# Performance work log

Measured on AMD Instinct MI355X. Metric: run time of the kernel, lower is better.

Reference implementation:

```python
import jax, jax.numpy as jnp
import numpy as np

B, N, C = 4, 2048, 512
H, D, L = 8, 64, 64  # num_heads, per-head dim, lunchbox_dim
SCALE = max(D, L) ** (-0.5)

def setup_inputs() -> dict:
    key = jax.random.key(0)
    k1, k2, k3, k4 = jax.random.split(key, 4)
    x = jax.random.normal(k1, (B, N, C), dtype=jnp.float32)
    v = jax.random.normal(k2, (N, H, L), dtype=jnp.float32) * (1.0 / np.sqrt(N))
    qkv = jax.random.normal(k3, (C, D * 2 * H), dtype=jnp.float32) * (1.0 / np.sqrt(C))
    proj = jax.random.normal(k4, (H * L, D), dtype=jnp.float32) * (1.0 / np.sqrt(H * L))
    return {"x": x, "v": v, "qkv": qkv, "proj": proj}

def reference(x, v, qkv, proj):
    # x: [B,N,C] -> [B,N,H,2,D]
    h = jnp.einsum('bnc,cd->bnd', x, qkv).reshape(B, N, H, 2, D)
    q = h[:, :, :, 0, :]  # [B,N,H,D]
    k = h[:, :, :, 1, :]  # [B,N,H,D]
    # attention scores [B,H,N,N]; NOTE: original code calls tf.nn.softmax but
    # discards the result, so no softmax is applied (faithful reproduction).
    attn = jnp.einsum('bnhd,bmhd->bhnm', q, k) * SCALE
    # contract with batch-independent lunchbox V: [B,H,N,N] x [N,H,L] -> [B,N,H,L]
    res = jnp.einsum('bhnm,mhl->bnhl', attn, v).reshape(B, N, H * L)
    out = jnp.einsum('bnc,cd->bnd', res, proj)  # [B,N,D]
    return out
```

## Files before the change

### kernel.cpp

```cpp
#include <hip/hip_runtime.h>
#include <hip/hip_bf16.h>


using f32x4 = __attribute__((ext_vector_type(4))) float;
using s16x8 = __attribute__((ext_vector_type(8))) short;

__device__ __forceinline__ unsigned short f2bf(float f) {
  unsigned int i;
  __builtin_memcpy(&i, &f, 4);
  unsigned int lsb = (i >> 16) & 1u;
  i += 0x7fffu + lsb;
  return (unsigned short)(i >> 16);
}
__device__ __forceinline__ float bf2f(unsigned short u) {
  unsigned int i = ((unsigned int)u) << 16;
  float f;
  __builtin_memcpy(&f, &i, 4);
  return f;
}
__device__ __forceinline__ ushort4 pk4(f32x4 a) {
  ushort4 u;
  u.x = f2bf(a[0]); u.y = f2bf(a[1]); u.z = f2bf(a[2]); u.w = f2bf(a[3]);
  return u;
}
__device__ __forceinline__ void async_cp16(const void* g, void* l) {
  __builtin_amdgcn_global_load_lds((const __attribute__((address_space(1))) void*)g,
                                   (__attribute__((address_space(3))) void*)l, 16, 0, 0);
}

__global__ void k_prep(const float* __restrict__ qkv, unsigned short* __restrict__ qkvT) {
  __shared__ float tile[32][33];
  const int idx = blockIdx.x;
  const int tid = threadIdx.x;
  const int j0 = (idx & 31) * 32;
  const int c0 = (idx >> 5) * 32;
  const int tx = tid & 31, ty = tid >> 5;
#pragma unroll
  for (int i = 0; i < 32; i += 8)
    tile[ty + i][tx] = qkv[(size_t)(c0 + ty + i) * 1024 + j0 + tx];
  __syncthreads();
  const int h = j0 >> 7, s = (j0 >> 6) & 1, d0 = j0 & 63;
  const int jp0 = s * 512 + h * 64 + d0;
#pragma unroll
  for (int i = 0; i < 32; i += 8)
    qkvT[(size_t)(jp0 + ty + i) * 512 + c0 + tx] = f2bf(tile[tx][ty + i]);
}

__global__ __launch_bounds__(512) void k_gemm1(
    const float* __restrict__ X,
    const unsigned short* __restrict__ Bt,
    unsigned short* __restrict__ Qws,
    unsigned short* __restrict__ Kws) {
  __shared__ unsigned short As[128 * 80];
  __shared__ unsigned short Bs[128 * 64];
  const int lin = blockIdx.x;
  const int wg = (lin & 7) * 64 + (lin >> 3);
  const int m0 = (wg >> 3) * 128;
  const int n0 = (wg & 7) * 128;
  const int tid = threadIdx.x;
  const int lane = tid & 63;
  const int wave = tid >> 6;
  const int wm = wave >> 1, wn = wave & 1;

  f32x4 acc[2][4] = {};

  const int arow_s = tid >> 4;
  const int acol_s = (tid & 15) * 4;
  const int rlane = lane >> 3;
  const int clane = (lane & 7) * 8;

  f32x4 areg[4];
#pragma unroll
  for (int i = 0; i < 4; ++i)
    areg[i] = *(const f32x4*)(X + (size_t)(m0 + i * 32 + arow_s) * 512 + acol_s);

  for (int kt = 0; kt < 512; kt += 64) {
    __syncthreads();
#pragma unroll
    for (int i = 0; i < 2; ++i)
      async_cp16(Bt + (size_t)(n0 + i * 64 + wave * 8 + rlane) * 512 + kt + clane,
                 Bs + (i * 64 + wave * 8) * 64);
#pragma unroll
    for (int i = 0; i < 4; ++i)
      *(ushort4*)(As + (i * 32 + arow_s) * 80 + acol_s) = pk4(areg[i]);
    __syncthreads();
    if (kt + 64 < 512) {
#pragma unroll
      for (int i = 0; i < 4; ++i)
        areg[i] = *(const f32x4*)(X + (size_t)(m0 + i * 32 + arow_s) * 512 + kt + 64 + acol_s);
    }
#pragma unroll
    for (int kk = 0; kk < 64; kk += 32) {
      s16x8 af[2], bfr[4];
#pragma unroll
      for (int i = 0; i < 2; ++i)
        af[i] = *(const s16x8*)(As + (wm * 32 + i * 16 + (lane & 15)) * 80 + kk + (lane >> 4) * 8);
#pragma unroll
      for (int j = 0; j < 4; ++j)
        bfr[j] = *(const s16x8*)(Bs + (wn * 64 + j * 16 + (lane & 15)) * 64 + kk + (lane >> 4) * 8);
#pragma unroll
      for (int i = 0; i < 2; ++i)
#pragma unroll
        for (int j = 0; j < 4; ++j)
          acc[i][j] = __builtin_amdgcn_mfma_f32_16x16x32_bf16(af[i], bfr[j], acc[i][j], 0, 0, 0);
    }
  }
  const int n_base = n0 + wn * 64;
#pragma unroll
  for (int i = 0; i < 2; ++i) {
    int grow = m0 + wm * 32 + i * 16 + (lane >> 4) * 4;
#pragma unroll
    for (int j = 0; j < 4; ++j) {
      int gcol = n_base + j * 16 + (lane & 15);
      unsigned short* dst;
      float scale;
      if (gcol < 512) { dst = Qws; scale = 0.125f; }
      else            { dst = Kws; gcol -= 512; scale = 1.0f; }
#pragma unroll
      for (int r = 0; r < 4; ++r)
        dst[(size_t)(grow + r) * 512 + gcol] = f2bf(acc[i][j][r] * scale);
    }
  }
}

__global__ void k_kv_partial(const unsigned short* __restrict__ Kws,
                             const float* __restrict__ v,
                             unsigned short* __restrict__ KVp) {
  const int wg = blockIdx.x;
  const int chunk = wg & 15;
  const int h = (wg >> 4) & 7;
  const int b = wg >> 7;
  __shared__ unsigned short Ks[128 * 64];
  __shared__ float Vs[128 * 64];
  const int tid = threadIdx.x;
  const int lane = tid & 63;
  const int wave = tid >> 6;
  const int n0 = chunk * 128;
  {
    const int r = wave * 32 + (lane >> 3);
    const int c = (lane & 7) * 8;
#pragma unroll
    for (int i = 0; i < 4; ++i)
      async_cp16(Kws + (size_t)(b * 2048 + n0 + r + i * 8) * 512 + h * 64 + c,
                 Ks + (wave * 32 + i * 8) * 64);
  }
  {
    const int r = wave * 32 + (lane >> 4);
    const int c = (lane & 15) * 4;
#pragma unroll
    for (int i = 0; i < 8; ++i)
      async_cp16(v + (size_t)(n0 + r + i * 4) * 512 + h * 64 + c,
                 Vs + (wave * 32 + i * 4) * 64);
  }
  __syncthreads();
  const int dq0 = (tid & 15) * 4;
  const int l0 = (tid >> 4) * 4;
  float acc[4][4] = {};
#pragma unroll 4
  for (int n = 0; n < 128; ++n) {
    ushort4 ku = *(const ushort4*)(Ks + n * 64 + dq0);
    f32x4 va = *(const f32x4*)(Vs + n * 64 + l0);
    float ka[4] = {bf2f(ku.x), bf2f(ku.y), bf2f(ku.z), bf2f(ku.w)};
#pragma unroll
    for (int a = 0; a < 4; ++a)
#pragma unroll
      for (int c = 0; c < 4; ++c)
        acc[a][c] += ka[a] * va[c];
  }
  unsigned short* dst = KVp + (size_t)wg * 4096;
#pragma unroll
  for (int a = 0; a < 4; ++a) {
    f32x4 o;
    o[0] = acc[a][0]; o[1] = acc[a][1]; o[2] = acc[a][2]; o[3] = acc[a][3];
    *(ushort4*)(dst + (dq0 + a) * 64 + l0) = pk4(o);
  }
}

__global__ void k_w(const unsigned short* __restrict__ KVp,
                    const float* __restrict__ proj,
                    unsigned short* __restrict__ WcatT) {
  const int blk = blockIdx.x;
  const int g = blk & 7;
  const int bh = blk >> 3;
  const int h = bh & 7;
  const int b = bh >> 3;
  __shared__ float kv[8 * 64];
  __shared__ float pj[64 * 64];
  const int tid = threadIdx.x;
  {
    const int e = tid * 2;
    const unsigned short* src = KVp + (size_t)bh * 16 * 4096 + g * 512 + e;
    float s0 = 0.f, s1 = 0.f;
#pragma unroll
    for (int c = 0; c < 16; ++c) {
      ushort2 t = *(const ushort2*)(src + c * 4096);
      s0 += bf2f(t.x); s1 += bf2f(t.y);
    }
    kv[e] = s0; kv[e + 1] = s1;
  }
#pragma unroll
  for (int j = 0; j < 16; ++j) {
    int e = tid + j * 256;
    pj[e] = proj[(size_t)h * 4096 + e];
  }
  __syncthreads();
  const int dout = tid & 63;
  const int dq0 = tid >> 6;
  float w0 = 0.f, w1 = 0.f;
  for (int l = 0; l < 64; ++l) {
    float p = pj[l * 64 + dout];
    w0 += kv[dq0 * 64 + l] * p;
    w1 += kv[(dq0 + 4) * 64 + l] * p;
  }
  const int dqb = h * 64 + g * 8;
  WcatT[(size_t)(b * 64 + dout) * 512 + dqb + dq0] = f2bf(w0);
  WcatT[(size_t)(b * 64 + dout) * 512 + dqb + dq0 + 4] = f2bf(w1);
}

__global__ __launch_bounds__(64) void k_gemm2(
    const unsigned short* __restrict__ Qws,
    const unsigned short* __restrict__ WcatT,
    float* __restrict__ out) {
  const int m0 = blockIdx.x * 16;
  const int lane = threadIdx.x;
  const unsigned short* Bb = WcatT + (size_t)(m0 >> 11) * 64 * 512;
  const int arow = lane & 15;
  const int koff = (lane >> 4) * 8;
  f32x4 acc[4] = {};
#pragma unroll
  for (int kk = 0; kk < 16; ++kk) {
    s16x8 af = *(const s16x8*)(Qws + (size_t)(m0 + arow) * 512 + kk * 32 + koff);
#pragma unroll
    for (int j = 0; j < 4; ++j) {
      s16x8 bf = *(const s16x8*)(Bb + (size_t)(j * 16 + arow) * 512 + kk * 32 + koff);
      acc[j] = __builtin_amdgcn_mfma_f32_16x16x32_bf16(af, bf, acc[j], 0, 0, 0);
    }
  }
  const int grow = m0 + (lane >> 4) * 4;
#pragma unroll
  for (int j = 0; j < 4; ++j) {
    int gcol = j * 16 + arow;
#pragma unroll
    for (int r = 0; r < 4; ++r)
      out[(size_t)(grow + r) * 64 + gcol] = acc[j][r];
  }
}

extern "C" void kernel_launch(void* const* d_in, const int* in_sizes, int n_in,
                              void* d_out, int out_size, void* d_ws, size_t ws_size,
                              hipStream_t stream) {
  const float* x    = (const float*)d_in[0];
  const float* v    = (const float*)d_in[1];
  const float* qkv  = (const float*)d_in[2];
  const float* proj = (const float*)d_in[3];
  float* out = (float*)d_out;

  char* ws = (char*)d_ws;
  unsigned short* qkvT = (unsigned short*)ws; ws += (size_t)1024 * 512 * 2;
  unsigned short* Qws  = (unsigned short*)ws; ws += (size_t)8192 * 512 * 2;
  unsigned short* Kws  = (unsigned short*)ws; ws += (size_t)8192 * 512 * 2;
  unsigned short* KVp  = (unsigned short*)ws; ws += (size_t)512 * 4096 * 2;
  unsigned short* Wc   = (unsigned short*)ws; ws += (size_t)4 * 64 * 512 * 2;

  hipLaunchKernelGGL(k_prep, dim3(512), dim3(256), 0, stream, qkv, qkvT);
  hipLaunchKernelGGL(k_gemm1, dim3(512), dim3(512), 0, stream, x, qkvT, Qws, Kws);
  hipLaunchKernelGGL(k_kv_partial, dim3(512), dim3(256), 0, stream, Kws, v, KVp);
  hipLaunchKernelGGL(k_w, dim3(256), dim3(256), 0, stream, KVp, proj, Wc);
  hipLaunchKernelGGL(k_gemm2, dim3(512), dim3(64), 0, stream, Qws, Wc, out);
}
```

Baseline: 112.1 us.

## Double-buffer B tile and prefetch two stages ahead in QKV GEMM

Restructures the k_gemm1 main loop so the bf16 B tile is double-buffered in LDS and loaded two k-steps ahead, while the fp32 A tile is also prefetched two steps ahead into registers. Explicit s_waitcnt vmcnt counts and raw s_barrier calls replace the pair of __syncthreads per iteration, so loads can overlap the MFMA work. This costs extra LDS for the second B buffer and relies on hand-counted vmcnt values, which must match the number of outstanding loads exactly for the result to be correct.

```diff
diff --git a/kernel.cpp b/kernel.cpp
--- a/kernel.cpp
+++ b/kernel.cpp
@@ -52,7 +52,7 @@
     unsigned short* __restrict__ Qws,
     unsigned short* __restrict__ Kws) {
   __shared__ unsigned short As[128 * 80];
-  __shared__ unsigned short Bs[128 * 64];
+  __shared__ unsigned short Bs[2][128 * 64];
   const int lin = blockIdx.x;
   const int wg = (lin & 7) * 64 + (lin >> 3);
   const int m0 = (wg >> 3) * 128;
@@ -69,26 +69,39 @@
   const int rlane = lane >> 3;
   const int clane = (lane & 7) * 8;
 
+#define ISSUE_B(buf, kt)                                                                \
+  {                                                                                     \
+    _Pragma("unroll") for (int i = 0; i < 2; ++i)                                       \
+        async_cp16(Bt + (size_t)(n0 + i * 64 + wave * 8 + rlane) * 512 + (kt) + clane,  \
+                   Bs[buf] + (i * 64 + wave * 8) * 64);                                 \
+  }
+#define LOAD_AREG(kt)                                                                   \
+  {                                                                                     \
+    _Pragma("unroll") for (int i = 0; i < 4; ++i)                                       \
+        areg[i] = *(const f32x4*)(X + (size_t)(m0 + i * 32 + arow_s) * 512 + (kt) +     \
+                                  acol_s);                                              \
+  }
+#define WRITE_AS()                                                                      \
+  {                                                                                     \
+    _Pragma("unroll") for (int i = 0; i < 4; ++i)                                       \
+        *(ushort4*)(As + (i * 32 + arow_s) * 80 + acol_s) = pk4(areg[i]);               \
+  }
+
   f32x4 areg[4];
-#pragma unroll
-  for (int i = 0; i < 4; ++i)
-    areg[i] = *(const f32x4*)(X + (size_t)(m0 + i * 32 + arow_s) * 512 + acol_s);
-
-  for (int kt = 0; kt < 512; kt += 64) {
-    __syncthreads();
-#pragma unroll
-    for (int i = 0; i < 2; ++i)
-      async_cp16(Bt + (size_t)(n0 + i * 64 + wave * 8 + rlane) * 512 + kt + clane,
-                 Bs + (i * 64 + wave * 8) * 64);
-#pragma unroll
-    for (int i = 0; i < 4; ++i)
-      *(ushort4*)(As + (i * 32 + arow_s) * 80 + acol_s) = pk4(areg[i]);
-    __syncthreads();
-    if (kt + 64 < 512) {
-#pragma unroll
-      for (int i = 0; i < 4; ++i)
-        areg[i] = *(const f32x4*)(X + (size_t)(m0 + i * 32 + arow_s) * 512 + kt + 64 + acol_s);
-    }
+  ISSUE_B(0, 0);
+  LOAD_AREG(0);
+  WRITE_AS();
+  ISSUE_B(1, 64);
+  LOAD_AREG(64);
+
+#pragma unroll
+  for (int t = 0; t < 8; ++t) {
+    if (t < 7)
+      asm volatile("s_waitcnt vmcnt(6) lgkmcnt(0)" ::: "memory");
+    else
+      asm volatile("s_waitcnt vmcnt(0) lgkmcnt(0)" ::: "memory");
+    __builtin_amdgcn_s_barrier();
+    __builtin_amdgcn_sched_barrier(0);
 #pragma unroll
     for (int kk = 0; kk < 64; kk += 32) {
       s16x8 af[2], bfr[4];
@@ -97,14 +110,26 @@
         af[i] = *(const s16x8*)(As + (wm * 32 + i * 16 + (lane & 15)) * 80 + kk + (lane >> 4) * 8);
 #pragma unroll
       for (int j = 0; j < 4; ++j)
-        bfr[j] = *(const s16x8*)(Bs + (wn * 64 + j * 16 + (lane & 15)) * 64 + kk + (lane >> 4) * 8);
+        bfr[j] = *(const s16x8*)(Bs[t & 1] + (wn * 64 + j * 16 + (lane & 15)) * 64 + kk + (lane >> 4) * 8);
 #pragma unroll
       for (int i = 0; i < 2; ++i)
 #pragma unroll
         for (int j = 0; j < 4; ++j)
           acc[i][j] = __builtin_amdgcn_mfma_f32_16x16x32_bf16(af[i], bfr[j], acc[i][j], 0, 0, 0);
     }
-  }
+    if (t < 7) {
+      __builtin_amdgcn_s_barrier();
+      WRITE_AS();
+      if (t < 6) {
+        ISSUE_B(t & 1, (t + 2) * 64);
+        LOAD_AREG((t + 2) * 64);
+      }
+    }
+  }
+#undef ISSUE_B
+#undef LOAD_AREG
+#undef WRITE_AS
+
   const int n_base = n0 + wn * 64;
 #pragma unroll
   for (int i = 0; i < 2; ++i) {
```

Measured after the change: 112.0 us. Within noise of the previous version (-0.1%).
